# Kernel tuning notes

Measured on AMD Instinct MI355X. Metric: run time of the kernel, lower is better.

The kernel has to match this reference:

```python
import jax, jax.numpy as jnp
import numpy as np

N_NODES = 50000
N_EDGES = 800000
NODE_DIM = 3
EDGE_DIM = 32
HIDDEN = 128
NUM_GRAPHS = 256


def _linear_init(key, fan_in, fan_out):
    # torch nn.Linear default: U(-1/sqrt(fan_in), 1/sqrt(fan_in))
    kw, kb = jax.random.split(key)
    bound = 1.0 / np.sqrt(fan_in)
    W = jax.random.uniform(kw, (fan_in, fan_out), jnp.float32, -bound, bound)
    b = jax.random.uniform(kb, (fan_out,), jnp.float32, -bound, bound)
    return W, b


def setup_inputs() -> dict:
    key = jax.random.key(0)
    ks = jax.random.split(key, 16)
    x = jax.random.normal(ks[0], (N_NODES, NODE_DIM), jnp.float32)
    edge_index = jax.random.randint(ks[1], (2, N_EDGES), 0, N_NODES, jnp.int64)
    edge_attr = jax.random.uniform(ks[2], (N_EDGES, EDGE_DIM), jnp.float32)
    batch = jnp.sort(jax.random.randint(ks[3], (N_NODES,), 0, NUM_GRAPHS, jnp.int64))

    # conv1: CGConv(channels=3, dim=32) -> lin_f, lin_s: (2*3+32) -> 3
    Wf1, bf1 = _linear_init(ks[4], 2 * NODE_DIM + EDGE_DIM, NODE_DIM)
    Ws1, bs1 = _linear_init(ks[5], 2 * NODE_DIM + EDGE_DIM, NODE_DIM)
    # node_proj: 3 -> 128
    Wp, bp = _linear_init(ks[6], NODE_DIM, HIDDEN)
    zin = 2 * HIDDEN + EDGE_DIM
    Wf_list, bf_list, Ws_list, bs_list = [], [], [], []
    for i in range(2):
        Wf, bf = _linear_init(ks[7 + i], zin, HIDDEN)
        Ws, bs = _linear_init(ks[9 + i], zin, HIDDEN)
        Wf_list.append(Wf); bf_list.append(bf); Ws_list.append(Ws); bs_list.append(bs)
    Wf_convs = jnp.stack(Wf_list); bf_convs = jnp.stack(bf_list)
    Ws_convs = jnp.stack(Ws_list); bs_convs = jnp.stack(bs_list)
    # fc1: 128 -> 128
    W1, b1 = _linear_init(ks[11], HIDDEN, HIDDEN)
    # 5 heads: 128 -> 1, stacked as (5, 128) and (5,)
    Wh_list, bh_list = [], []
    for i in range(5):
        Wh, bh = _linear_init(jax.random.fold_in(ks[12], i), HIDDEN, 1)
        Wh_list.append(Wh[:, 0]); bh_list.append(bh[0])
    W_heads = jnp.stack(Wh_list)  # (5, 128)
    b_heads = jnp.stack(bh_list)  # (5,)

    return dict(x=x, edge_index=edge_index, edge_attr=edge_attr, batch=batch,
                Wf1=Wf1, bf1=bf1, Ws1=Ws1, bs1=bs1, Wp=Wp, bp=bp,
                Wf_convs=Wf_convs, bf_convs=bf_convs, Ws_convs=Ws_convs, bs_convs=bs_convs,
                W1=W1, b1=b1, W_heads=W_heads, b_heads=b_heads)


def _cgconv(x, src, dst, edge_attr, Wf, bf, Ws, bs):
    # PyG CGConv: z_ij = [x_i || x_j || e_ij], messages aggregated to i (dst)
    z = jnp.concatenate([x[dst], x[src], edge_attr], axis=-1)  # [E, 2C+D]
    msg = jax.nn.sigmoid(z @ Wf + bf) * jax.nn.softplus(z @ Ws + bs)  # [E, C]
    agg = jax.ops.segment_sum(msg, dst, num_segments=x.shape[0])
    return x + agg


def reference(x, edge_index, edge_attr, batch,
              Wf1, bf1, Ws1, bs1, Wp, bp,
              Wf_convs, bf_convs, Ws_convs, bs_convs,
              W1, b1, W_heads, b_heads):
    src, dst = edge_index[0], edge_index[1]
    h = _cgconv(x, src, dst, edge_attr, Wf1, bf1, Ws1, bs1)
    h = jax.nn.relu(h @ Wp + bp)
    for l in range(Wf_convs.shape[0]):
        h = _cgconv(h, src, dst, edge_attr, Wf_convs[l], bf_convs[l], Ws_convs[l], bs_convs[l])
        h = jax.nn.relu(h)
    # global mean pool over graphs
    sums = jax.ops.segment_sum(h, batch, num_segments=NUM_GRAPHS)
    counts = jax.ops.segment_sum(jnp.ones((h.shape[0],), h.dtype), batch, num_segments=NUM_GRAPHS)
    g = sums / jnp.maximum(counts, 1.0)[:, None]  # [G, H]
    g = jax.nn.relu(g @ W1 + b1)
    # 5 heads stacked -> [G, 5] (columns: volume, band_gap, formation_energy, density, bulk_modulus)
    out = g @ W_heads.T + b_heads
    return out
```

## Files before the change

kernel.cpp:

```cpp
#include <hip/hip_runtime.h>
#include <hip/hip_bf16.h>
#include <math.h>

#define N_NODES 50000
#define N_EDGES 800000
#define NODE_DIM 3
#define EDGE_DIM 32
#define HIDDEN 128
#define NUM_GRAPHS 256
#define ZIN (2*HIDDEN + EDGE_DIM)
#define NPAD 50176

#define LOG2E 1.44269504088896f
#define LN2   0.69314718055995f

typedef __attribute__((ext_vector_type(8))) short short8;
typedef __attribute__((ext_vector_type(4))) float f32x4;

__device__ __forceinline__ unsigned short f2bf(float x) {
    unsigned u = __float_as_uint(x);
    u += 0x7FFFu + ((u >> 16) & 1u);
    return (unsigned short)(u >> 16);
}
__device__ __forceinline__ float bf_lo(unsigned u) { return __uint_as_float(u << 16); }
__device__ __forceinline__ float bf_hi(unsigned u) { return __uint_as_float(u & 0xFFFF0000u); }

__global__ __launch_bounds__(256) void conv1_sorted_kernel(
    const float* __restrict__ x, const float* __restrict__ EA,
    const int4* __restrict__ epack,
    const float* __restrict__ Wf1, const float* __restrict__ bf1,
    const float* __restrict__ Ws1, const float* __restrict__ bs1,
    float* __restrict__ agg0)
{
    __shared__ float WfL[38*3], WsL[38*3], bfL[3], bsL[3];
    __shared__ float msgL[256*5];
    __shared__ int   pdL[256];

    if (threadIdx.x < 114) {
        WfL[threadIdx.x] = Wf1[threadIdx.x] * LOG2E;
        WsL[threadIdx.x] = Ws1[threadIdx.x] * LOG2E;
    }
    if (threadIdx.x < 3) {
        bfL[threadIdx.x] = bf1[threadIdx.x] * LOG2E;
        bsL[threadIdx.x] = bs1[threadIdx.x] * LOG2E;
    }
    __syncthreads();

    const int p = blockIdx.x * 256 + threadIdx.x;
    int4 e = epack[p];
    const int eid = e.x, s = e.y, d = e.z;
    pdL[threadIdx.x] = d;

    float z[38];
    z[0] = x[d*3+0]; z[1] = x[d*3+1]; z[2] = x[d*3+2];
    z[3] = x[s*3+0]; z[4] = x[s*3+1]; z[5] = x[s*3+2];
    const float4* ep = (const float4*)(EA + (size_t)eid * EDGE_DIM);
    #pragma unroll
    for (int q = 0; q < 8; ++q) {
        float4 v = ep[q];
        z[6+4*q+0] = v.x; z[6+4*q+1] = v.y; z[6+4*q+2] = v.z; z[6+4*q+3] = v.w;
    }
    float f[3], g[3];
    #pragma unroll
    for (int c = 0; c < 3; ++c) { f[c] = bfL[c]; g[c] = bsL[c]; }
    #pragma unroll
    for (int j = 0; j < 38; ++j) {
        #pragma unroll
        for (int c = 0; c < 3; ++c) {
            f[c] += z[j] * WfL[j*3+c];
            g[c] += z[j] * WsL[j*3+c];
        }
    }
    #pragma unroll
    for (int c = 0; c < 3; ++c) {
        float sig = __builtin_amdgcn_rcpf(1.0f + __builtin_amdgcn_exp2f(-f[c]));
        float sp  = __builtin_amdgcn_logf(1.0f + __builtin_amdgcn_exp2f(g[c]));
        msgL[threadIdx.x*5 + c] = sig * sp;
    }
    __syncthreads();

    if (threadIdx.x < 48) {
        const int c   = threadIdx.x % 3;
        const int seg = threadIdx.x / 3;
        const int base = seg * 16;
        float acc = 0.0f;
        int cur = pdL[base];
        #pragma unroll 4
        for (int i = 0; i < 16; ++i) {
            int dd = pdL[base + i];
            float v = msgL[(base + i)*5 + c];
            if (dd != cur) {
                atomicAdd(agg0 + (size_t)cur*3 + c, acc);
                acc = 0.0f; cur = dd;
            }
            acc += v;
        }
        atomicAdd(agg0 + (size_t)cur*3 + c, acc);
    }
}

__global__ __launch_bounds__(256) void proj_kernel(
    const float* __restrict__ x, const float* __restrict__ agg0,
    const float* __restrict__ Wp, const float* __restrict__ bp,
    float* __restrict__ H)
{
    int idx = blockIdx.x * 256 + threadIdx.x;
    if (idx >= N_NODES * HIDDEN) return;
    int n = idx >> 7, c = idx & 127;
    float h0 = fmaf(agg0[n*3+0], LN2, x[n*3+0]);
    float h1 = fmaf(agg0[n*3+1], LN2, x[n*3+1]);
    float h2 = fmaf(agg0[n*3+2], LN2, x[n*3+2]);
    float v = bp[c] + h0*Wp[0*128+c] + h1*Wp[1*128+c] + h2*Wp[2*128+c];
    H[idx] = fmaxf(v, 0.0f);
}

__global__ __launch_bounds__(256) void hist_kernel(
    const int* __restrict__ ei, int* __restrict__ hist)
{
    int e = blockIdx.x * 256 + threadIdx.x;
    if (e < N_EDGES) atomicAdd(&hist[ei[N_EDGES + e]], 1);
}

__global__ __launch_bounds__(256) void scanA_kernel(
    const int* __restrict__ hist, int* __restrict__ cursor, int* __restrict__ btot)
{
    __shared__ int tmp[256];
    int t = threadIdx.x;
    int i = blockIdx.x * 256 + t;
    int v = hist[i];
    tmp[t] = v;
    __syncthreads();
    #pragma unroll
    for (int off = 1; off < 256; off <<= 1) {
        int y = (t >= off) ? tmp[t - off] : 0;
        __syncthreads();
        if (t >= off) tmp[t] += y;
        __syncthreads();
    }
    cursor[i] = tmp[t] - v;
    if (t == 255) btot[blockIdx.x] = tmp[t];
}

__global__ __launch_bounds__(256) void scanB_kernel(int* __restrict__ btot)
{
    __shared__ int tmp[256];
    int t = threadIdx.x;
    int v = btot[t];
    tmp[t] = v;
    __syncthreads();
    #pragma unroll
    for (int off = 1; off < 256; off <<= 1) {
        int y = (t >= off) ? tmp[t - off] : 0;
        __syncthreads();
        if (t >= off) tmp[t] += y;
        __syncthreads();
    }
    btot[t] = tmp[t] - v;
}

__global__ __launch_bounds__(256) void scatter_kernel(
    const int* __restrict__ ei, int* __restrict__ cursor,
    const int* __restrict__ btot, int4* __restrict__ epack)
{
    int e = blockIdx.x * 256 + threadIdx.x;
    if (e >= N_EDGES) return;
    int s = ei[e];
    int d = ei[N_EDGES + e];
    int p = atomicAdd(&cursor[d], 1) + btot[d >> 8];
    epack[p] = make_int4(e, s, d, 0);
}

__global__ __launch_bounds__(256) void repack_all_kernel(
    const float* __restrict__ Wf, const float* __restrict__ Ws,
    unsigned short* __restrict__ Bfrag, unsigned short* __restrict__ BE)
{
    int idx = blockIdx.x * 256 + threadIdx.x;
    if (idx < 2*32*4*64) {
        int lane = idx & 63;
        int kc   = (idx >> 6) & 3;
        int nt   = (idx >> 8) & 31;
        int l    = idx >> 13;
        const float* wf  = Wf + (size_t)l * ZIN * HIDDEN;
        const float* wsp = Ws + (size_t)l * ZIN * HIDDEN;
        int n = nt*16 + (lane & 15);
        int half = n >> 8;
        int within = n & 255;
        int cc = within >> 1;
        int t = within & 1;
        const float* W = t ? wsp : wf;
        unsigned short vals[8];
        #pragma unroll
        for (int j = 0; j < 8; ++j) {
            int k = kc*32 + (lane >> 4)*8 + j;
            vals[j] = f2bf(W[(size_t)(half*128 + k)*128 + cc] * LOG2E);
        }
        *(short8*)(Bfrag + (size_t)idx * 8) = *(short8*)vals;
    } else if (idx < 2*32*4*64 + 2*16*64) {
        int i2 = idx - 2*32*4*64;
        int lane = i2 & 63;
        int nt   = (i2 >> 6) & 15;
        int l    = i2 >> 10;
        const float* W = ((nt & 8) ? Ws : Wf) + (size_t)l * ZIN * HIDDEN + 256*128;
        int c = (nt & 7)*16 + (lane & 15);
        unsigned short vals[8];
        #pragma unroll
        for (int j = 0; j < 8; ++j) {
            int k = (lane >> 4)*8 + j;
            vals[j] = f2bf(W[(size_t)k*128 + c] * LOG2E);
        }
        *(short8*)(BE + (size_t)i2 * 8) = *(short8*)vals;
    }
}

__global__ __launch_bounds__(256) void gemm_mfma(
    const float* __restrict__ H, const float* __restrict__ aggIn,
    const unsigned short* __restrict__ Bfrag,
    const float* __restrict__ bf, const float* __restrict__ bs,
    unsigned short* __restrict__ Pb)
{
    const int lane = threadIdx.x & 63;
    const int wave = threadIdx.x >> 6;
    const int m    = lane & 15;
    const int quad = lane >> 4;
    const int rowA = blockIdx.y * 64 + wave * 16 + m;
    const int colBase = blockIdx.x * 256;

    const float* hrow = H + (size_t)rowA * 128;
    short8 a[4];
    #pragma unroll
    for (int kc = 0; kc < 4; ++kc) {
        float4 v0 = *(const float4*)(hrow + kc*32 + quad*8);
        float4 v1 = *(const float4*)(hrow + kc*32 + quad*8 + 4);
        if (aggIn) {
            const float* arow = aggIn + (size_t)rowA * 128;
            float4 a0 = *(const float4*)(arow + kc*32 + quad*8);
            float4 a1 = *(const float4*)(arow + kc*32 + quad*8 + 4);
        v0.x = fmaxf(fmaf(a0.x, LN2, v0.x), 0.f); v0.y = fmaxf(fmaf(a0.y, LN2, v0.y), 0.f);
        v0.z = fmaxf(fmaf(a0.z, LN2, v0.z), 0.f); v0.w = fmaxf(fmaf(a0.w, LN2, v0.w), 0.f);
        v1.x = fmaxf(fmaf(a1.x, LN2, v1.x), 0.f); v1.y = fmaxf(fmaf(a1.y, LN2, v1.y), 0.f);
        v1.z = fmaxf(fmaf(a1.z, LN2, v1.z), 0.f); v1.w = fmaxf(fmaf(a1.w, LN2, v1.w), 0.f);
        }
        unsigned short t[8];
        t[0]=f2bf(v0.x); t[1]=f2bf(v0.y); t[2]=f2bf(v0.z); t[3]=f2bf(v0.w);
        t[4]=f2bf(v1.x); t[5]=f2bf(v1.y); t[6]=f2bf(v1.z); t[7]=f2bf(v1.w);
        a[kc] = *(short8*)t;
    }

    f32x4 acc[16];
    #pragma unroll
    for (int nt = 0; nt < 16; ++nt) {
        float bias = 0.0f;
        if (colBase == 0) {
            int col = nt*16 + m;
            bias = ((col & 1) ? bs[col >> 1] : bf[col >> 1]) * LOG2E;
        }
        acc[nt] = (f32x4){bias, bias, bias, bias};
    }

    #pragma unroll
    for (int nt = 0; nt < 16; ++nt) {
        int ntg = (colBase >> 4) + nt;
        const unsigned short* bp = Bfrag + ((size_t)(ntg*4) * 64 + lane) * 8;
        #pragma unroll
        for (int kc = 0; kc < 4; ++kc) {
            short8 b = *(const short8*)(bp + (size_t)kc * 64 * 8);
            acc[nt] = __builtin_amdgcn_mfma_f32_16x16x32_bf16(a[kc], b, acc[nt], 0, 0, 0);
        }
    }

    const int rowC = blockIdx.y * 64 + wave * 16 + quad * 4;
    #pragma unroll
    for (int nt = 0; nt < 16; ++nt) {
        int col = colBase + nt*16 + m;
        #pragma unroll
        for (int r = 0; r < 4; ++r) {
            int row = rowC + r;
            if (row < N_NODES) Pb[(size_t)row * 512 + col] = f2bf(acc[nt][r]);
        }
    }
}

__global__ __launch_bounds__(256, 8) void edge_kernel(
    const unsigned short* __restrict__ Pb, const float* __restrict__ EA,
    const int4* __restrict__ epack,
    const unsigned short* __restrict__ BE,
    float* __restrict__ agg)
{
    __shared__ float msgL[64*68];
    __shared__ int pdL[64];
    __shared__ unsigned bmaskL[2];

    if (threadIdx.x < 64) {
        const int t = threadIdx.x;
        int d = epack[blockIdx.x*64 + t].z;
        pdL[t] = d;
        bool b = (t & 15) ? (d != pdL[t-1]) : false;
        unsigned long long bal = __ballot(b);
        if (t == 0) { bmaskL[0] = (unsigned)bal; bmaskL[1] = (unsigned)(bal >> 32); }
    }

    const int lane = threadIdx.x & 63;
    const int wave = threadIdx.x >> 6;
    const int m    = lane & 15;
    const int quad = lane >> 4;
    const int p0   = blockIdx.x * 64 + wave * 16;

    int eid = epack[p0 + m].x;
    const float* ea = EA + (size_t)eid * EDGE_DIM + quad*8;
    float4 v0 = *(const float4*)ea;
    float4 v1 = *(const float4*)(ea + 4);
    unsigned short t[8];
    t[0]=f2bf(v0.x); t[1]=f2bf(v0.y); t[2]=f2bf(v0.z); t[3]=f2bf(v0.w);
    t[4]=f2bf(v1.x); t[5]=f2bf(v1.y); t[6]=f2bf(v1.z); t[7]=f2bf(v1.w);
    short8 a = *(short8*)t;

    const unsigned short* pdp[4];
    const unsigned short* psp[4];
    #pragma unroll
    for (int r = 0; r < 4; ++r) {
        int4 e = epack[p0 + quad*4 + r];
        pdp[r] = Pb + (size_t)e.z * 512 + 2*m;
        psp[r] = Pb + (size_t)e.y * 512 + 256 + 2*m;
    }

    const short8* BEv = (const short8*)BE;
    const int chunk  = wave*4 + quad;
    const int c2  = threadIdx.x & 63;
    const int seg = threadIdx.x >> 6;

    #pragma unroll
    for (int half = 0; half < 2; ++half) {
        #pragma unroll
        for (int nt4 = 0; nt4 < 4; ++nt4) {
            const int nt = half*4 + nt4;
            short8 bF = BEv[nt*64 + lane];
            short8 bS = BEv[(nt+8)*64 + lane];
            f32x4 accF, accS;
            #pragma unroll
            for (int r = 0; r < 4; ++r) {
                unsigned pd = *(const unsigned*)(pdp[r] + nt*32);
                unsigned ps = *(const unsigned*)(psp[r] + nt*32);
                accF[r] = bf_lo(pd) + bf_lo(ps);
                accS[r] = bf_hi(pd) + bf_hi(ps);
            }
            f32x4 qf = __builtin_amdgcn_mfma_f32_16x16x32_bf16(a, bF, accF, 0, 0, 0);
            f32x4 qs = __builtin_amdgcn_mfma_f32_16x16x32_bf16(a, bS, accS, 0, 0, 0);
            float4 mv;
            #pragma unroll
            for (int r = 0; r < 4; ++r) {
                float sig = __builtin_amdgcn_rcpf(1.0f + __builtin_amdgcn_exp2f(-qf[r]));
                float sp  = __builtin_amdgcn_logf(1.0f + __builtin_amdgcn_exp2f(qs[r]));
                ((float*)&mv)[r] = sig * sp;
            }
            const int row = nt4*16 + m;
            const int chunkp = (chunk + 2*m) & 15;
            *(float4*)&msgL[row*68 + chunkp*4] = mv;
        }
        __syncthreads();

        unsigned mfull = bmaskL[seg >> 1];
        unsigned msk = (unsigned)__builtin_amdgcn_readfirstlane(
            (int)((mfull >> ((seg & 1) * 16)) & 0xFFFEu));
        const int swz = 2*(c2 & 15);
        const float* rowp = &msgL[c2*68];
        float* aggc = agg + half*64 + c2;
        const int base = seg*16;
        float acc = 0.0f;
        bool inside = false;
        #pragma unroll
        for (int jj = 0; jj < 4; ++jj) {
            const int ch = seg*4 + jj;
            const float4 v4 = *(const float4*)&rowp[((ch + swz) & 15)*4];
            #pragma unroll
            for (int k = 0; k < 4; ++k) {
                if (msk & 1u) {
                    float* dp = &aggc[(size_t)pdL[base + jj*4 + k - 1] * HIDDEN];
                    if (inside) *dp = acc; else atomicAdd(dp, acc);
                    acc = 0.0f; inside = true;
                }
                msk >>= 1;
                acc += ((const float*)&v4)[k];
            }
        }
        atomicAdd(&aggc[(size_t)pdL[base + 15] * HIDDEN], acc);
        if (half == 0) __syncthreads();
    }
}

__global__ __launch_bounds__(128) void pool_kernel(
    const float* __restrict__ H, const float* __restrict__ agg1,
    const float* __restrict__ agg2, const int* __restrict__ batch,
    float* __restrict__ gsum, float* __restrict__ gcnt)
{
    const int c = threadIdx.x;
    const int n0 = blockIdx.x * 32;
    float acc = 0.0f;
    int cur = -1;
    for (int i = 0; i < 32; ++i) {
        int n = n0 + i;
        if (n >= N_NODES) break;
        int g = batch[n];
        if (g != cur) {
            if (cur >= 0) atomicAdd(gsum + (size_t)cur * HIDDEN + c, acc);
            cur = g; acc = 0.0f;
        }
        size_t ix = (size_t)n * HIDDEN + c;
        float h = fmaxf(fmaf(agg2[ix], LN2, fmaxf(fmaf(agg1[ix], LN2, H[ix]), 0.0f)), 0.0f);
        acc += h;
    }
    if (cur >= 0) atomicAdd(gsum + (size_t)cur * HIDDEN + c, acc);

    if (c == 0) {
        int curg = -1; float run = 0.0f;
        for (int i = 0; i < 32; ++i) {
            int n = n0 + i;
            if (n >= N_NODES) break;
            int g = batch[n];
            if (g != curg) {
                if (curg >= 0) atomicAdd(gcnt + curg, run);
                curg = g; run = 0.0f;
            }
            run += 1.0f;
        }
        if (curg >= 0) atomicAdd(gcnt + curg, run);
    }
}

__global__ __launch_bounds__(128) void head_kernel(
    const float* __restrict__ gsum, const float* __restrict__ gcnt,
    const float* __restrict__ W1, const float* __restrict__ b1,
    const float* __restrict__ Wh, const float* __restrict__ bh,
    float* __restrict__ out)
{
    __shared__ float gavg[128];
    __shared__ float g1[128];
    const int g = blockIdx.x, c = threadIdx.x;
    float cnt = fmaxf(gcnt[g], 1.0f);
    gavg[c] = gsum[(size_t)g * HIDDEN + c] / cnt;
    __syncthreads();
    float acc = b1[c];
    for (int k = 0; k < 128; ++k) acc += gavg[k] * W1[k*128 + c];
    g1[c] = fmaxf(acc, 0.0f);
    __syncthreads();
    if (c < 5) {
        float o = bh[c];
        for (int k = 0; k < 128; ++k) o += g1[k] * Wh[c*128 + k];
        out[(size_t)g * 5 + c] = o;
    }
}

extern "C" void kernel_launch(void* const* d_in, const int* in_sizes, int n_in,
                              void* d_out, int out_size, void* d_ws, size_t ws_size,
                              hipStream_t stream) {
    const float* x        = (const float*)d_in[0];
    const int*   ei       = (const int*)  d_in[1];
    const float* EA       = (const float*)d_in[2];
    const int*   batch    = (const int*)  d_in[3];
    const float* Wf1      = (const float*)d_in[4];
    const float* bf1      = (const float*)d_in[5];
    const float* Ws1      = (const float*)d_in[6];
    const float* bs1      = (const float*)d_in[7];
    const float* Wp       = (const float*)d_in[8];
    const float* bp       = (const float*)d_in[9];
    const float* Wf_convs = (const float*)d_in[10];
    const float* bf_convs = (const float*)d_in[11];
    const float* Ws_convs = (const float*)d_in[12];
    const float* bs_convs = (const float*)d_in[13];
    const float* W1       = (const float*)d_in[14];
    const float* b1       = (const float*)d_in[15];
    const float* W_heads  = (const float*)d_in[16];
    const float* b_heads  = (const float*)d_in[17];
    float* out = (float*)d_out;

    float* ws = (float*)d_ws;
    float* agg0 = ws + 0;
    float* H    = ws + 150016;
    unsigned short* Pb = (unsigned short*)(ws + 6550016);
    float* agg1 = ws + 19350016;
    float* agg2 = ws + 25750016;
    unsigned short* Bfrag = (unsigned short*)(ws + 32150016);
    unsigned short* BE    = (unsigned short*)(ws + 32215552);
    float* gsum = ws + 32223744;
    float* gcnt = ws + 32256512;
    int* hist   = (int*)(ws + 32257024);
    int* cursor = (int*)(ws + 32307200);
    int* btot   = (int*)(ws + 32357376);
    int4* epack = (int4*)(ws + 32357632);

    hipMemsetAsync(hist, 0, (size_t)NPAD * sizeof(int), stream);
    hist_kernel<<<(N_EDGES + 255)/256, 256, 0, stream>>>(ei, hist);
    scanA_kernel<<<NPAD/256, 256, 0, stream>>>(hist, cursor, btot);
    scanB_kernel<<<1, 256, 0, stream>>>(btot);
    scatter_kernel<<<(N_EDGES + 255)/256, 256, 0, stream>>>(ei, cursor, btot, epack);

    hipMemsetAsync(agg0, 0, (size_t)N_NODES * 3 * sizeof(float), stream);
    conv1_sorted_kernel<<<N_EDGES/256, 256, 0, stream>>>(x, EA, epack, Wf1, bf1, Ws1, bs1, agg0);
    proj_kernel<<<(N_NODES*HIDDEN + 255)/256, 256, 0, stream>>>(x, agg0, Wp, bp, H);
    repack_all_kernel<<<(2*32*4*64 + 2*16*64 + 255)/256, 256, 0, stream>>>(
        Wf_convs, Ws_convs, Bfrag, BE);

    hipMemsetAsync(agg1, 0, (size_t)2 * N_NODES * HIDDEN * sizeof(float), stream);

    dim3 ggrid(2, (N_NODES + 63)/64);
    gemm_mfma<<<ggrid, 256, 0, stream>>>(H, nullptr, Bfrag, bf_convs, bs_convs, Pb);
    edge_kernel<<<N_EDGES/64, 256, 0, stream>>>(Pb, EA, epack, BE, agg1);
    gemm_mfma<<<ggrid, 256, 0, stream>>>(H, agg1, Bfrag + (size_t)32*4*64*8,
                                         bf_convs + HIDDEN, bs_convs + HIDDEN, Pb);
    edge_kernel<<<N_EDGES/64, 256, 0, stream>>>(Pb, EA, epack, BE + (size_t)16*64*8, agg2);

    hipMemsetAsync(gsum, 0, (size_t)(NUM_GRAPHS * HIDDEN + NUM_GRAPHS) * sizeof(float), stream);
    pool_kernel<<<(N_NODES + 31)/32, 128, 0, stream>>>(H, agg1, agg2, batch, gsum, gcnt);
    head_kernel<<<NUM_GRAPHS, 128, 0, stream>>>(gsum, gcnt, W1, b1, W_heads, b_heads, out);
}
```

Before: 616.2 us.

## Fuse projection into first GEMM, pre-sort bf16 edge attrs, merge setup kernels

New measurement: 608.5 us. Within noise of the previous version (-1.2%).

```diff
diff --git a/kernel.cpp b/kernel.cpp
--- a/kernel.cpp
+++ b/kernel.cpp
@@ -30,7 +30,7 @@
     const int4* __restrict__ epack,
     const float* __restrict__ Wf1, const float* __restrict__ bf1,
     const float* __restrict__ Ws1, const float* __restrict__ bs1,
-    float* __restrict__ agg0)
+    float* __restrict__ agg0, unsigned short* __restrict__ EAb)
 {
     __shared__ float WfL[38*3], WsL[38*3], bfL[3], bsL[3];
     __shared__ float msgL[256*5];
@@ -60,6 +60,18 @@
         float4 v = ep[q];
         z[6+4*q+0] = v.x; z[6+4*q+1] = v.y; z[6+4*q+2] = v.z; z[6+4*q+3] = v.w;
     }
+
+    if (EAb) {
+        unsigned short vals[32];
+        #pragma unroll
+        for (int j = 0; j < 32; ++j) vals[j] = f2bf(z[6+j]);
+        unsigned short* dst = EAb + (size_t)p * 32;
+        *(short8*)(dst + 0)  = *(short8*)(vals + 0);
+        *(short8*)(dst + 8)  = *(short8*)(vals + 8);
+        *(short8*)(dst + 16) = *(short8*)(vals + 16);
+        *(short8*)(dst + 24) = *(short8*)(vals + 24);
+    }
+
     float f[3], g[3];
     #pragma unroll
     for (int c = 0; c < 3; ++c) { f[c] = bfL[c]; g[c] = bsL[c]; }
@@ -99,82 +111,15 @@
     }
 }
 
-__global__ __launch_bounds__(256) void proj_kernel(
-    const float* __restrict__ x, const float* __restrict__ agg0,
-    const float* __restrict__ Wp, const float* __restrict__ bp,
-    float* __restrict__ H)
-{
-    int idx = blockIdx.x * 256 + threadIdx.x;
-    if (idx >= N_NODES * HIDDEN) return;
-    int n = idx >> 7, c = idx & 127;
-    float h0 = fmaf(agg0[n*3+0], LN2, x[n*3+0]);
-    float h1 = fmaf(agg0[n*3+1], LN2, x[n*3+1]);
-    float h2 = fmaf(agg0[n*3+2], LN2, x[n*3+2]);
-    float v = bp[c] + h0*Wp[0*128+c] + h1*Wp[1*128+c] + h2*Wp[2*128+c];
-    H[idx] = fmaxf(v, 0.0f);
-}
-
-__global__ __launch_bounds__(256) void hist_kernel(
-    const int* __restrict__ ei, int* __restrict__ hist)
+__global__ __launch_bounds__(256) void hist_repack_kernel(
+    const int* __restrict__ ei, int* __restrict__ hist,
+    const float* __restrict__ Wf, const float* __restrict__ Ws,
+    unsigned short* __restrict__ Bfrag, unsigned short* __restrict__ BE)
 {
     int e = blockIdx.x * 256 + threadIdx.x;
     if (e < N_EDGES) atomicAdd(&hist[ei[N_EDGES + e]], 1);
-}
-
-__global__ __launch_bounds__(256) void scanA_kernel(
-    const int* __restrict__ hist, int* __restrict__ cursor, int* __restrict__ btot)
-{
-    __shared__ int tmp[256];
-    int t = threadIdx.x;
-    int i = blockIdx.x * 256 + t;
-    int v = hist[i];
-    tmp[t] = v;
-    __syncthreads();
-    #pragma unroll
-    for (int off = 1; off < 256; off <<= 1) {
-        int y = (t >= off) ? tmp[t - off] : 0;
-        __syncthreads();
-        if (t >= off) tmp[t] += y;
-        __syncthreads();
-    }
-    cursor[i] = tmp[t] - v;
-    if (t == 255) btot[blockIdx.x] = tmp[t];
-}
-
-__global__ __launch_bounds__(256) void scanB_kernel(int* __restrict__ btot)
-{
-    __shared__ int tmp[256];
-    int t = threadIdx.x;
-    int v = btot[t];
-    tmp[t] = v;
-    __syncthreads();
-    #pragma unroll
-    for (int off = 1; off < 256; off <<= 1) {
-        int y = (t >= off) ? tmp[t - off] : 0;
-        __syncthreads();
-        if (t >= off) tmp[t] += y;
-        __syncthreads();
-    }
-    btot[t] = tmp[t] - v;
-}
-
-__global__ __launch_bounds__(256) void scatter_kernel(
-    const int* __restrict__ ei, int* __restrict__ cursor,
-    const int* __restrict__ btot, int4* __restrict__ epack)
-{
-    int e = blockIdx.x * 256 + threadIdx.x;
-    if (e >= N_EDGES) return;
-    int s = ei[e];
-    int d = ei[N_EDGES + e];
-    int p = atomicAdd(&cursor[d], 1) + btot[d >> 8];
-    epack[p] = make_int4(e, s, d, 0);
-}
-
-__global__ __launch_bounds__(256) void repack_all_kernel(
-    const float* __restrict__ Wf, const float* __restrict__ Ws,
-    unsigned short* __restrict__ Bfrag, unsigned short* __restrict__ BE)
-{
-    int idx = blockIdx.x * 256 + threadIdx.x;
+
+    int idx = e;
     if (idx < 2*32*4*64) {
         int lane = idx & 63;
         int kc   = (idx >> 6) & 3;
@@ -212,6 +157,137 @@
     }
 }
 
+__global__ __launch_bounds__(256) void scanA_kernel(
+    const int* __restrict__ hist, int* __restrict__ cursor, int* __restrict__ btot)
+{
+    __shared__ int tmp[256];
+    int t = threadIdx.x;
+    int i = blockIdx.x * 256 + t;
+    int v = hist[i];
+    tmp[t] = v;
+    __syncthreads();
+    #pragma unroll
+    for (int off = 1; off < 256; off <<= 1) {
+        int y = (t >= off) ? tmp[t - off] : 0;
+        __syncthreads();
+        if (t >= off) tmp[t] += y;
+        __syncthreads();
+    }
+    cursor[i] = tmp[t] - v;
+    if (t == 255) btot[blockIdx.x] = tmp[t];
+}
+
+__global__ __launch_bounds__(256) void scanB_kernel(int* __restrict__ btot)
+{
+    __shared__ int tmp[256];
+    int t = threadIdx.x;
+    int v = btot[t];
+    tmp[t] = v;
+    __syncthreads();
+    #pragma unroll
+    for (int off = 1; off < 256; off <<= 1) {
+        int y = (t >= off) ? tmp[t - off] : 0;
+        __syncthreads();
+        if (t >= off) tmp[t] += y;
+        __syncthreads();
+    }
+    btot[t] = tmp[t] - v;
+}
+
+__global__ __launch_bounds__(256) void scatter_kernel(
+    const int* __restrict__ ei, int* __restrict__ cursor,
+    const int* __restrict__ btot, int4* __restrict__ epack)
+{
+    int e = blockIdx.x * 256 + threadIdx.x;
+    if (e >= N_EDGES) return;
+    int s = ei[e];
+    int d = ei[N_EDGES + e];
+    int p = atomicAdd(&cursor[d], 1) + btot[d >> 8];
+    epack[p] = make_int4(e, s, d, 0);
+}
+
+__global__ __launch_bounds__(256) void gemm0_fused_kernel(
+    const float* __restrict__ x, const float* __restrict__ agg0,
+    const float* __restrict__ Wp, const float* __restrict__ bp,
+    const unsigned short* __restrict__ Bfrag,
+    const float* __restrict__ bf, const float* __restrict__ bs,
+    unsigned short* __restrict__ Pb, float* __restrict__ H)
+{
+    __shared__ float WpL[384], bpL[128];
+    WpL[threadIdx.x] = Wp[threadIdx.x];
+    if (threadIdx.x < 128) {
+        WpL[256 + threadIdx.x] = Wp[256 + threadIdx.x];
+        bpL[threadIdx.x] = bp[threadIdx.x];
+    }
+    __syncthreads();
+
+    const int lane = threadIdx.x & 63;
+    const int wave = threadIdx.x >> 6;
+    const int m    = lane & 15;
+    const int quad = lane >> 4;
+    const int rowA = blockIdx.y * 64 + wave * 16 + m;
+    const int rowX = rowA < N_NODES ? rowA : N_NODES - 1;
+    const int colBase = blockIdx.x * 256;
+
+    float h0 = fmaf(agg0[rowX*3+0], LN2, x[rowX*3+0]);
+    float h1 = fmaf(agg0[rowX*3+1], LN2, x[rowX*3+1]);
+    float h2 = fmaf(agg0[rowX*3+2], LN2, x[rowX*3+2]);
+
+    short8 a[4];
+    #pragma unroll
+    for (int kc = 0; kc < 4; ++kc) {
+        float vv[8];
+        unsigned short t[8];
+        #pragma unroll
+        for (int i = 0; i < 8; ++i) {
+            int col = kc*32 + quad*8 + i;
+            float v = bpL[col] + h0*WpL[col] + h1*WpL[128+col] + h2*WpL[256+col];
+            v = fmaxf(v, 0.0f);
+            vv[i] = v;
+            t[i] = f2bf(v);
+        }
+        a[kc] = *(short8*)t;
+        if (colBase == 0 && rowA < N_NODES) {
+            float* hp = H + (size_t)rowA * 128 + kc*32 + quad*8;
+            *(float4*)hp       = make_float4(vv[0], vv[1], vv[2], vv[3]);
+            *(float4*)(hp + 4) = make_float4(vv[4], vv[5], vv[6], vv[7]);
+        }
+    }
+
+    f32x4 acc[16];
+    #pragma unroll
+    for (int nt = 0; nt < 16; ++nt) {
+        float bias = 0.0f;
+        if (colBase == 0) {
+            int col = nt*16 + m;
+            bias = ((col & 1) ? bs[col >> 1] : bf[col >> 1]) * LOG2E;
+        }
+        acc[nt] = (f32x4){bias, bias, bias, bias};
+    }
+
+    #pragma unroll
+    for (int nt = 0; nt < 16; ++nt) {
+        int ntg = (colBase >> 4) + nt;
+        const unsigned short* bpf = Bfrag + ((size_t)(ntg*4) * 64 + lane) * 8;
+        #pragma unroll
+        for (int kc = 0; kc < 4; ++kc) {
+            short8 b = *(const short8*)(bpf + (size_t)kc * 64 * 8);
+            acc[nt] = __builtin_amdgcn_mfma_f32_16x16x32_bf16(a[kc], b, acc[nt], 0, 0, 0);
+        }
+    }
+
+    const int rowC = blockIdx.y * 64 + wave * 16 + quad * 4;
+    #pragma unroll
+    for (int nt = 0; nt < 16; ++nt) {
+        int col = colBase + nt*16 + m;
+        #pragma unroll
+        for (int r = 0; r < 4; ++r) {
+            int row = rowC + r;
+            if (row < N_NODES) Pb[(size_t)row * 512 + col] = f2bf(acc[nt][r]);
+        }
+    }
+}
+
 __global__ __launch_bounds__(256) void gemm_mfma(
     const float* __restrict__ H, const float* __restrict__ aggIn,
     const unsigned short* __restrict__ Bfrag,
@@ -226,20 +302,18 @@
     const int colBase = blockIdx.x * 256;
 
     const float* hrow = H + (size_t)rowA * 128;
+    const float* arow = aggIn + (size_t)rowA * 128;
     short8 a[4];
     #pragma unroll
     for (int kc = 0; kc < 4; ++kc) {
         float4 v0 = *(const float4*)(hrow + kc*32 + quad*8);
         float4 v1 = *(const float4*)(hrow + kc*32 + quad*8 + 4);
-        if (aggIn) {
-            const float* arow = aggIn + (size_t)rowA * 128;
-            float4 a0 = *(const float4*)(arow + kc*32 + quad*8);
-            float4 a1 = *(const float4*)(arow + kc*32 + quad*8 + 4);
+        float4 a0 = *(const float4*)(arow + kc*32 + quad*8);
+        float4 a1 = *(const float4*)(arow + kc*32 + quad*8 + 4);
         v0.x = fmaxf(fmaf(a0.x, LN2, v0.x), 0.f); v0.y = fmaxf(fmaf(a0.y, LN2, v0.y), 0.f);
         v0.z = fmaxf(fmaf(a0.z, LN2, v0.z), 0.f); v0.w = fmaxf(fmaf(a0.w, LN2, v0.w), 0.f);
         v1.x = fmaxf(fmaf(a1.x, LN2, v1.x), 0.f); v1.y = fmaxf(fmaf(a1.y, LN2, v1.y), 0.f);
         v1.z = fmaxf(fmaf(a1.z, LN2, v1.z), 0.f); v1.w = fmaxf(fmaf(a1.w, LN2, v1.w), 0.f);
-        }
         unsigned short t[8];
         t[0]=f2bf(v0.x); t[1]=f2bf(v0.y); t[2]=f2bf(v0.z); t[3]=f2bf(v0.w);
         t[4]=f2bf(v1.x); t[5]=f2bf(v1.y); t[6]=f2bf(v1.z); t[7]=f2bf(v1.w);
@@ -282,6 +356,7 @@
 
 __global__ __launch_bounds__(256, 8) void edge_kernel(
     const unsigned short* __restrict__ Pb, const float* __restrict__ EA,
+    const unsigned short* __restrict__ EAb,
     const int4* __restrict__ epack,
     const unsigned short* __restrict__ BE,
     float* __restrict__ agg)
@@ -294,7 +369,7 @@
         const int t = threadIdx.x;
         int d = epack[blockIdx.x*64 + t].z;
         pdL[t] = d;
-        bool b = (t & 15) ? (d != pdL[t-1]) : false;
+        bool b = (t & 31) ? (d != pdL[t-1]) : false;
         unsigned long long bal = __ballot(b);
         if (t == 0) { bmaskL[0] = (unsigned)bal; bmaskL[1] = (unsigned)(bal >> 32); }
     }
@@ -305,14 +380,19 @@
     const int quad = lane >> 4;
     const int p0   = blockIdx.x * 64 + wave * 16;
 
-    int eid = epack[p0 + m].x;
-    const float* ea = EA + (size_t)eid * EDGE_DIM + quad*8;
-    float4 v0 = *(const float4*)ea;
-    float4 v1 = *(const float4*)(ea + 4);
-    unsigned short t[8];
-    t[0]=f2bf(v0.x); t[1]=f2bf(v0.y); t[2]=f2bf(v0.z); t[3]=f2bf(v0.w);
-    t[4]=f2bf(v1.x); t[5]=f2bf(v1.y); t[6]=f2bf(v1.z); t[7]=f2bf(v1.w);
-    short8 a = *(short8*)t;
+    short8 a;
+    if (EAb) {
+        a = *(const short8*)(EAb + (size_t)(p0 + m) * 32 + quad*8);
+    } else {
+        int eid = epack[p0 + m].x;
+        const float* ea = EA + (size_t)eid * EDGE_DIM + quad*8;
+        float4 v0 = *(const float4*)ea;
+        float4 v1 = *(const float4*)(ea + 4);
+        unsigned short t[8];
+        t[0]=f2bf(v0.x); t[1]=f2bf(v0.y); t[2]=f2bf(v0.z); t[3]=f2bf(v0.w);
+        t[4]=f2bf(v1.x); t[5]=f2bf(v1.y); t[6]=f2bf(v1.z); t[7]=f2bf(v1.w);
+        a = *(short8*)t;
+    }
 
     const unsigned short* pdp[4];
     const unsigned short* psp[4];
@@ -326,7 +406,7 @@
     const short8* BEv = (const short8*)BE;
     const int chunk  = wave*4 + quad;
     const int c2  = threadIdx.x & 63;
-    const int seg = threadIdx.x >> 6;
+    const int seg = (threadIdx.x >> 6) & 1;
 
     #pragma unroll
     for (int half = 0; half < 2; ++half) {
@@ -358,31 +438,31 @@
         }
         __syncthreads();
 
-        unsigned mfull = bmaskL[seg >> 1];
-        unsigned msk = (unsigned)__builtin_amdgcn_readfirstlane(
-            (int)((mfull >> ((seg & 1) * 16)) & 0xFFFEu));
-        const int swz = 2*(c2 & 15);
-        const float* rowp = &msgL[c2*68];
-        float* aggc = agg + half*64 + c2;
-        const int base = seg*16;
-        float acc = 0.0f;
-        bool inside = false;
-        #pragma unroll
-        for (int jj = 0; jj < 4; ++jj) {
-            const int ch = seg*4 + jj;
-            const float4 v4 = *(const float4*)&rowp[((ch + swz) & 15)*4];
+        if (threadIdx.x < 128) {
+            unsigned msk = (unsigned)__builtin_amdgcn_readfirstlane((int)bmaskL[seg]);
+            const int swz = 2*(c2 & 15);
+            const float* rowp = &msgL[c2*68];
+            float* aggc = agg + half*64 + c2;
+            const int base = seg*32;
+            float acc = 0.0f;
+            bool inside = false;
             #pragma unroll
-            for (int k = 0; k < 4; ++k) {
-                if (msk & 1u) {
-                    float* dp = &aggc[(size_t)pdL[base + jj*4 + k - 1] * HIDDEN];
-                    if (inside) *dp = acc; else atomicAdd(dp, acc);
-                    acc = 0.0f; inside = true;
+            for (int jj = 0; jj < 8; ++jj) {
+                const int ch = seg*8 + jj;
+                const float4 v4 = *(const float4*)&rowp[((ch + swz) & 15)*4];
+                #pragma unroll
+                for (int k = 0; k < 4; ++k) {
+                    if (msk & 1u) {
+                        float* dp = &aggc[(size_t)pdL[base + jj*4 + k - 1] * HIDDEN];
+                        if (inside) *dp = acc; else atomicAdd(dp, acc);
+                        acc = 0.0f; inside = true;
+                    }
+                    msk >>= 1;
+                    acc += ((const float*)&v4)[k];
                 }
-                msk >>= 1;
-                acc += ((const float*)&v4)[k];
             }
-        }
-        atomicAdd(&aggc[(size_t)pdL[base + 15] * HIDDEN], acc);
+            atomicAdd(&aggc[(size_t)pdL[base + 31] * HIDDEN], acc);
+        }
         if (half == 0) __syncthreads();
     }
 }
@@ -473,11 +553,11 @@
     float* out = (float*)d_out;
 
     float* ws = (float*)d_ws;
-    float* agg0 = ws + 0;
-    float* H    = ws + 150016;
-    unsigned short* Pb = (unsigned short*)(ws + 6550016);
-    float* agg1 = ws + 19350016;
-    float* agg2 = ws + 25750016;
+    float* H    = ws + 0;
+    unsigned short* Pb = (unsigned short*)(ws + 6400000);
+    float* agg1 = ws + 19200000;
+    float* agg2 = ws + 25600000;
+    float* agg0 = ws + 32000000;
     unsigned short* Bfrag = (unsigned short*)(ws + 32150016);
     unsigned short* BE    = (unsigned short*)(ws + 32215552);
     float* gsum = ws + 32223744;
@@ -486,29 +566,32 @@
     int* cursor = (int*)(ws + 32307200);
     int* btot   = (int*)(ws + 32357376);
     int4* epack = (int4*)(ws + 32357632);
+    unsigned short* EAb = (unsigned short*)(ws + 35557632);
+    const size_t need_eab = (size_t)(35557632 + 12800000) * 4;
+    unsigned short* EAb_use = (ws_size >= need_eab) ? EAb : (unsigned short*)nullptr;
 
     hipMemsetAsync(hist, 0, (size_t)NPAD * sizeof(int), stream);
-    hist_kernel<<<(N_EDGES + 255)/256, 256, 0, stream>>>(ei, hist);
+    hipMemsetAsync(agg1, 0, (size_t)(2 * N_NODES * HIDDEN + 150016) * sizeof(float), stream);
+    hipMemsetAsync(gsum, 0, (size_t)(NUM_GRAPHS * HIDDEN + NUM_GRAPHS) * sizeof(float), stream);
+
+    hist_repack_kernel<<<(N_EDGES + 255)/256, 256, 0, stream>>>(
+        ei, hist, Wf_convs, Ws_convs, Bfrag, BE);
     scanA_kernel<<<NPAD/256, 256, 0, stream>>>(hist, cursor, btot);
     scanB_kernel<<<1, 256, 0, stream>>>(btot);
     scatter_kernel<<<(N_EDGES + 255)/256, 256, 0, stream>>>(ei, cursor, btot, epack);
 
-    hipMemsetAsync(agg0, 0, (size_t)N_NODES * 3 * sizeof(float), stream);
-    conv1_sorted_kernel<<<N_EDGES/256, 256, 0, stream>>>(x, EA, epack, Wf1, bf1, Ws1, bs1, agg0);
-    proj_kernel<<<(N_NODES*HIDDEN + 255)/256, 256, 0, stream>>>(x, agg0, Wp, bp, H);
-    repack_all_kernel<<<(2*32*4*64 + 2*16*64 + 255)/256, 256, 0, stream>>>(
-        Wf_convs, Ws_convs, Bfrag, BE);
-
-    hipMemsetAsync(agg1, 0, (size_t)2 * N_NODES * HIDDEN * sizeof(float), stream);
+    conv1_sorted_kernel<<<N_EDGES/256, 256, 0, stream>>>(
+        x, EA, epack, Wf1, bf1, Ws1, bs1, agg0, EAb_use);
 
     dim3 ggrid(2, (N_NODES + 63)/64);
-    gemm_mfma<<<ggrid, 256, 0, stream>>>(H, nullptr, Bfrag, bf_convs, bs_convs, Pb);
-    edge_kernel<<<N_EDGES/64, 256, 0, stream>>>(Pb, EA, epack, BE, agg1);
+    gemm0_fused_kernel<<<ggrid, 256, 0, stream>>>(
+        x, agg0, Wp, bp, Bfrag, bf_convs, bs_convs, Pb, H);
+    edge_kernel<<<N_EDGES/64, 256, 0, stream>>>(Pb, EA, EAb_use, epack, BE, agg1);
     gemm_mfma<<<ggrid, 256, 0, stream>>>(H, agg1, Bfrag + (size_t)32*4*64*8,
                                          bf_convs + HIDDEN, bs_convs + HIDDEN, Pb);
-    edge_kernel<<<N_EDGES/64, 256, 0, stream>>>(Pb, EA, epack, BE + (size_t)16*64*8, agg2);
-
-    hipMemsetAsync(gsum, 0, (size_t)(NUM_GRAPHS * HIDDEN + NUM_GRAPHS) * sizeof(float), stream);
+    edge_kernel<<<N_EDGES/64, 256, 0, stream>>>(Pb, EA, EAb_use, epack,
+                                                BE + (size_t)16*64*8, agg2);
+
     pool_kernel<<<(N_NODES + 31)/32, 128, 0, stream>>>(H, agg1, agg2, batch, gsum, gcnt);
     head_kernel<<<NUM_GRAPHS, 128, 0, stream>>>(gsum, gcnt, W1, b1, W_heads, b_heads, out);
 }
```
